# Performance work log

Hardware: AMD Instinct MI355X
Metric: run time of the kernel (lower is better)

## Reference

```python
import jax, jax.numpy as jnp
import numpy as np

E, TOP_K, D, H = 8, 2, 1024, 2048


def setup_inputs() -> dict:
    key = jax.random.key(0)
    ks = jax.random.split(key, 9)
    s = 0.02
    inputs = jax.random.normal(ks[0], (2, 2048, D), dtype=jnp.float32)
    gate_w = jax.random.normal(ks[1], (E, D), dtype=jnp.float32) * s  # Linear(d->E), no bias
    W0 = jax.random.normal(ks[2], (E, D, H), dtype=jnp.float32) * s
    b0 = jnp.zeros((E, H), dtype=jnp.float32)
    W1 = jax.random.normal(ks[3], (E, D, H), dtype=jnp.float32) * s
    b1 = jnp.zeros((E, H), dtype=jnp.float32)
    W2 = jax.random.normal(ks[4], (E, H, D), dtype=jnp.float32) * s
    b2 = jnp.zeros((E, D), dtype=jnp.float32)
    return {"inputs": inputs, "gate_w": gate_w, "W0": W0, "b0": b0,
            "W1": W1, "b1": b1, "W2": W2, "b2": b2}


def reference(inputs, gate_w, W0, b0, W1, b1, W2, b2):
    shp = inputs.shape
    x = inputs.reshape(-1, shp[-1])                      # [T, D]
    T = x.shape[0]
    logits = x @ gate_w.T                                # [T, E]
    w, sel = jax.lax.top_k(logits, TOP_K)                # [T, K]
    w = jax.nn.softmax(w, axis=-1)
    # dense combine weights [T, E]; top-k indices are distinct per row
    combine = jnp.zeros((T, E), dtype=x.dtype).at[
        jnp.arange(T)[:, None], sel].set(w)
    # per-expert SwiGLU FFN, evaluated densely, combined with (mostly zero) weights
    h0 = jnp.einsum('td,edh->eth', x, W0) + b0[:, None, :]
    h1 = jnp.einsum('td,edh->eth', x, W1) + b1[:, None, :]
    y = jnp.einsum('eth,ehd->etd', h0 * jax.nn.silu(h1), W2) + b2[:, None, :]
    out = jnp.einsum('te,etd->td', combine, y)           # [T, D]
    return out.reshape(shp)
```

## Files before the change

### kernel.cpp

```cpp
#include <hip/hip_runtime.h>
#include <hip/hip_bf16.h>
#include <cstdint>


#define E_ 8
#define D_ 1024
#define H_ 2048
#define T_ 4096

typedef __attribute__((ext_vector_type(8))) __bf16 bf16x8;
typedef __attribute__((ext_vector_type(4))) float f32x4;
typedef unsigned short u16;
typedef __attribute__((ext_vector_type(4))) u16 u16x4;

__device__ __forceinline__ u16 f2b(float f) {
    union { float f; unsigned int u; } v; v.f = f;
    unsigned int u = v.u;
    return (u16)((u + 0x7FFFu + ((u >> 16) & 1u)) >> 16);
}

__device__ __forceinline__ float b2f(u16 v) {
    union { unsigned int u; float f; } x; x.u = (unsigned int)v << 16; return x.f;
}

__device__ __forceinline__ void gld16(const void* g, void* l) {
    __builtin_amdgcn_global_load_lds((const __attribute__((address_space(1))) void*)g,
                                     (__attribute__((address_space(3))) void*)l, 16, 0, 0);
}

__global__ void k_gate(const float* __restrict__ x, const float* __restrict__ gw,
                       int* __restrict__ cnt2, int4* __restrict__ tslot,
                       float2* __restrict__ twgt, u16* __restrict__ xb) {
    __shared__ float gws[E_ * D_];
    int tid = threadIdx.x;
#pragma unroll
    for (int p = 0; p < 8; ++p) {
        int i = (p * 256 + tid) * 4;
        *(float4*)&gws[i] = *(const float4*)&gw[i];
    }
    __syncthreads();
    int wid = tid >> 6, lane = tid & 63;
    int t = blockIdx.x * 4 + wid;
    int chunk = blockIdx.x & 63;
    const float* xr = x + (size_t)t * D_;
    float part[E_];
#pragma unroll
    for (int e = 0; e < E_; ++e) part[e] = 0.f;
#pragma unroll
    for (int i = 0; i < 4; ++i) {
        int d = i * 256 + lane * 4;
        float4 xv = *(const float4*)(xr + d);
        u16x4 o;
        o[0] = f2b(xv.x); o[1] = f2b(xv.y); o[2] = f2b(xv.z); o[3] = f2b(xv.w);
        *(u16x4*)(xb + (size_t)t * D_ + d) = o;
#pragma unroll
        for (int e = 0; e < E_; ++e) {
            float4 g = *(const float4*)&gws[e * D_ + d];
            part[e] += xv.x * g.x + xv.y * g.y + xv.z * g.z + xv.w * g.w;
        }
    }
#pragma unroll
    for (int off = 32; off >= 1; off >>= 1) {
#pragma unroll
        for (int e = 0; e < E_; ++e) part[e] += __shfl_xor(part[e], off);
    }
    if (lane == 0) {
        int e0 = 0; float m0 = part[0];
#pragma unroll
        for (int e = 1; e < E_; ++e) if (part[e] > m0) { m0 = part[e]; e0 = e; }
        int e1 = -1; float m1 = -3.4e38f;
#pragma unroll
        for (int e = 0; e < E_; ++e) if (e != e0 && part[e] > m1) { m1 = part[e]; e1 = e; }
        float sx = __expf(m1 - m0);
        float w0 = 1.f / (1.f + sx);
        float w1 = sx / (1.f + sx);
        int lp0 = atomicAdd(&cnt2[chunk * 16 + e0], 1);
        int lp1 = atomicAdd(&cnt2[chunk * 16 + e1], 1);
        tslot[t] = make_int4(e0, lp0, e1, lp1);
        twgt[t] = make_float2(w0, w1);
    }
}

__global__ void k_scan2(const int* __restrict__ cnt2, int* __restrict__ chunk_off,
                        int* __restrict__ cnt, int* __restrict__ offs) {
    __shared__ int totals[E_];
    int e = threadIdx.x >> 6, lane = threadIdx.x & 63;
    int v = cnt2[lane * 16 + e];
    int incl = v;
#pragma unroll
    for (int d = 1; d < 64; d <<= 1) {
        int u = __shfl_up(incl, d);
        if (lane >= d) incl += u;
    }
    int excl = incl - v;
    if (lane == 63) totals[e] = incl;
    __syncthreads();
    chunk_off[lane * 8 + e] = excl;
    if (lane == 0) {
        int off_e = 0;
        for (int q = 0; q < e; ++q) off_e += totals[q];
        offs[e] = off_e; cnt[e] = totals[e];
    }
}

__global__ void k_fixup(const int* __restrict__ chunk_off, int4* __restrict__ tslot,
                        int* __restrict__ tok) {
    int t = blockIdx.x * 256 + threadIdx.x;
    int chunk = (t >> 2) & 63;
    int4 r = tslot[t];
    int s0 = chunk_off[chunk * 8 + r.x] + r.y;
    int s1 = chunk_off[chunk * 8 + r.z] + r.w;
    tok[r.x * T_ + s0] = t;
    tok[r.z * T_ + s1] = t;
    tslot[t] = make_int4(r.x, s0, r.z, s1);
}

__global__ void k_transpose_all(const float* __restrict__ W0, const float* __restrict__ W1,
                                const float* __restrict__ W2, u16* __restrict__ w0t,
                                u16* __restrict__ w1t, u16* __restrict__ w2t) {
    __shared__ float tile[64][67];
    int z = blockIdx.z, which = z >> 3, e = z & 7;
    const float* src; u16* dst; int R, C, c0, r0;
    if (which == 0)      { src = W0 + (size_t)e * D_ * H_; dst = w0t + (size_t)e * D_ * H_;
                           R = D_; C = H_; c0 = blockIdx.x * 64; r0 = blockIdx.y * 64; }
    else if (which == 1) { src = W1 + (size_t)e * D_ * H_; dst = w1t + (size_t)e * D_ * H_;
                           R = D_; C = H_; c0 = blockIdx.x * 64; r0 = blockIdx.y * 64; }
    else                 { src = W2 + (size_t)e * H_ * D_; dst = w2t + (size_t)e * H_ * D_;
                           R = H_; C = D_; c0 = blockIdx.y * 64; r0 = blockIdx.x * 64; }
    int tc4 = (threadIdx.x & 15) * 4, tr = threadIdx.x >> 4;
#pragma unroll
    for (int p = 0; p < 4; ++p) {
        float4 v = *(const float4*)(src + (size_t)(r0 + tr + 16 * p) * C + c0 + tc4);
        tile[tr + 16 * p][tc4 + 0] = v.x;
        tile[tr + 16 * p][tc4 + 1] = v.y;
        tile[tr + 16 * p][tc4 + 2] = v.z;
        tile[tr + 16 * p][tc4 + 3] = v.w;
    }
    __syncthreads();
    int r4 = (threadIdx.x & 15) * 4, tc = threadIdx.x >> 4;
#pragma unroll
    for (int p = 0; p < 4; ++p) {
        int c = tc + 16 * p;
        u16x4 o;
#pragma unroll
        for (int j = 0; j < 4; ++j) o[j] = f2b(tile[r4 + j][c]);
        *(u16x4*)(dst + (size_t)(c0 + c) * R + r0 + r4) = o;
    }
}

__launch_bounds__(256, 2)
__global__ void k_gemm1(const u16* __restrict__ xb, const u16* __restrict__ w0t,
                        const u16* __restrict__ w1t, const float* __restrict__ b0,
                        const float* __restrict__ b1, const int* __restrict__ tok,
                        const int* __restrict__ cnt, const int* __restrict__ offs,
                        u16* __restrict__ gbuf) {
    int e = blockIdx.z, rt = blockIdx.y, ct = blockIdx.x;
    int cN = cnt[e];
    if (rt * 128 >= cN) return;
    __shared__ u16 lds[16384];
    char* ldsB = (char*)lds;
    int tid = threadIdx.x, wid = tid >> 6, lane = tid & 63;
    int wm = wid >> 1, wn = wid & 1;
    const int* tokE = tok + e * T_;
    const u16* w0e = w0t + (size_t)e * H_ * D_;
    const u16* w1e = w1t + (size_t)e * H_ * D_;

    size_t aoff[4]; int adst[4];
#pragma unroll
    for (int p = 0; p < 4; ++p) {
        int cid = p * 256 + tid, r = cid >> 3, c = cid & 7;
        int cc = c ^ (r & 7);
        int tk = tokE[min(rt * 128 + r, cN - 1)];
        aoff[p] = (size_t)tk * D_ + cc * 8;
        adst[p] = (p * 256 + wid * 64) * 16;
    }
    size_t boff[2]; int bdst[2];
#pragma unroll
    for (int p = 0; p < 2; ++p) {
        int cid = p * 256 + tid, n = cid >> 3, c = cid & 7;
        int cc = c ^ (n & 7);
        boff[p] = (size_t)(ct * 64 + n) * D_ + cc * 8;
        bdst[p] = (p * 256 + wid * 64) * 16;
    }

    f32x4 acc0[4][2], acc1[4][2];
#pragma unroll
    for (int m = 0; m < 4; ++m)
#pragma unroll
        for (int n = 0; n < 2; ++n) { acc0[m][n] = (f32x4)0.f; acc1[m][n] = (f32x4)0.f; }

    for (int kt = 0; kt < D_ / 64; ++kt) {
        int k0 = kt * 64;
        __syncthreads();
#pragma unroll
        for (int p = 0; p < 4; ++p) gld16(xb + aoff[p] + k0, ldsB + adst[p]);
#pragma unroll
        for (int p = 0; p < 2; ++p) gld16(w0e + boff[p] + k0, ldsB + 16384 + bdst[p]);
#pragma unroll
        for (int p = 0; p < 2; ++p) gld16(w1e + boff[p] + k0, ldsB + 24576 + bdst[p]);
        __syncthreads();
#pragma unroll
        for (int ks = 0; ks < 2; ++ks) {
            int kc = ks * 4 + (lane >> 4);
            bf16x8 af[4], b0f[2], b1f[2];
#pragma unroll
            for (int m = 0; m < 4; ++m) {
                int row = wm * 64 + m * 16 + (lane & 15);
                af[m] = *(const bf16x8*)(ldsB + row * 128 + ((kc ^ (row & 7)) << 4));
            }
#pragma unroll
            for (int n = 0; n < 2; ++n) {
                int nr = wn * 32 + n * 16 + (lane & 15);
                int so = (kc ^ (nr & 7)) << 4;
                b0f[n] = *(const bf16x8*)(ldsB + 16384 + nr * 128 + so);
                b1f[n] = *(const bf16x8*)(ldsB + 24576 + nr * 128 + so);
            }
#pragma unroll
            for (int m = 0; m < 4; ++m)
#pragma unroll
                for (int n = 0; n < 2; ++n) {
                    acc0[m][n] = __builtin_amdgcn_mfma_f32_16x16x32_bf16(af[m], b0f[n], acc0[m][n], 0, 0, 0);
                    acc1[m][n] = __builtin_amdgcn_mfma_f32_16x16x32_bf16(af[m], b1f[n], acc1[m][n], 0, 0, 0);
                }
        }
    }
    int off_e = offs[e];
    const float* b0e = b0 + e * H_;
    const float* b1e = b1 + e * H_;
#pragma unroll
    for (int n = 0; n < 2; ++n) {
        int hc = ct * 64 + wn * 32 + n * 16 + (lane & 15);
        float bb0 = b0e[hc], bb1 = b1e[hc];
#pragma unroll
        for (int m = 0; m < 4; ++m)
#pragma unroll
            for (int i = 0; i < 4; ++i) {
                int row = wm * 64 + m * 16 + (lane >> 4) * 4 + i;
                int idx = rt * 128 + row;
                if (idx < cN) {
                    float h0 = acc0[m][n][i] + bb0;
                    float h1 = acc1[m][n][i] + bb1;
                    float g = h0 * h1 / (1.f + __expf(-h1));
                    gbuf[(size_t)(off_e + idx) * H_ + hc] = f2b(g);
                }
            }
    }
}

__launch_bounds__(256, 2)
__global__ void k_gemm2(const u16* __restrict__ gbuf, const u16* __restrict__ w2t,
                        const float* __restrict__ b2, const int* __restrict__ cnt,
                        const int* __restrict__ offs, u16* __restrict__ yb) {
    int e = blockIdx.z, rt = blockIdx.y, ct = blockIdx.x;
    int cN = cnt[e];
    if (rt * 128 >= cN) return;
    __shared__ u16 lds[16384];
    char* ldsB = (char*)lds;
    int tid = threadIdx.x, wid = tid >> 6, lane = tid & 63;
    int wm = wid >> 1, wn = wid & 1;
    int off_e = offs[e];
    const u16* Ag = gbuf + (size_t)(off_e + rt * 128) * H_;
    const u16* Bw = w2t + (size_t)e * D_ * H_ + (size_t)(ct * 128) * H_;

    size_t soff[4]; int sdst[4];
#pragma unroll
    for (int p = 0; p < 4; ++p) {
        int cid = p * 256 + tid, r = cid >> 3, c = cid & 7;
        int cc = c ^ (r & 7);
        soff[p] = (size_t)r * H_ + cc * 8;
        sdst[p] = (p * 256 + wid * 64) * 16;
    }
    f32x4 acc[4][4];
#pragma unroll
    for (int m = 0; m < 4; ++m)
#pragma unroll
        for (int n = 0; n < 4; ++n) acc[m][n] = (f32x4)0.f;

    for (int kt = 0; kt < H_ / 64; ++kt) {
        int k0 = kt * 64;
        __syncthreads();
#pragma unroll
        for (int p = 0; p < 4; ++p) gld16(Ag + soff[p] + k0, ldsB + sdst[p]);
#pragma unroll
        for (int p = 0; p < 4; ++p) gld16(Bw + soff[p] + k0, ldsB + 16384 + sdst[p]);
        __syncthreads();
#pragma unroll
        for (int ks = 0; ks < 2; ++ks) {
            int kc = ks * 4 + (lane >> 4);
            bf16x8 af[4], bfr[4];
#pragma unroll
            for (int m = 0; m < 4; ++m) {
                int row = wm * 64 + m * 16 + (lane & 15);
                af[m] = *(const bf16x8*)(ldsB + row * 128 + ((kc ^ (row & 7)) << 4));
            }
#pragma unroll
            for (int n = 0; n < 4; ++n) {
                int nr = wn * 64 + n * 16 + (lane & 15);
                bfr[n] = *(const bf16x8*)(ldsB + 16384 + nr * 128 + ((kc ^ (nr & 7)) << 4));
            }
#pragma unroll
            for (int m = 0; m < 4; ++m)
#pragma unroll
                for (int n = 0; n < 4; ++n)
                    acc[m][n] = __builtin_amdgcn_mfma_f32_16x16x32_bf16(af[m], bfr[n], acc[m][n], 0, 0, 0);
        }
    }
    const float* b2e = b2 + e * D_;
#pragma unroll
    for (int m = 0; m < 4; ++m)
#pragma unroll
        for (int i = 0; i < 4; ++i) {
            int row = wm * 64 + m * 16 + (lane >> 4) * 4 + i;
            int idx = rt * 128 + row;
            if (idx < cN) {
#pragma unroll
                for (int n = 0; n < 4; ++n) {
                    int dc = ct * 128 + wn * 64 + n * 16 + (lane & 15);
                    yb[(size_t)(off_e + idx) * D_ + dc] = f2b(acc[m][n][i] + b2e[dc]);
                }
            }
        }
}

__global__ void k_combine(const u16* __restrict__ yb, const int4* __restrict__ tslot,
                          const float2* __restrict__ twgt, const int* __restrict__ offs,
                          float* __restrict__ out) {
    int t = blockIdx.x, d4 = threadIdx.x * 4;
    int4 s = tslot[t];
    float2 w = twgt[t];
    const u16* y0 = yb + (size_t)(offs[s.x] + s.y) * D_ + d4;
    const u16* y1 = yb + (size_t)(offs[s.z] + s.w) * D_ + d4;
    u16x4 a = *(const u16x4*)y0;
    u16x4 b = *(const u16x4*)y1;
    float4 o;
    o.x = w.x * b2f(a[0]) + w.y * b2f(b[0]);
    o.y = w.x * b2f(a[1]) + w.y * b2f(b[1]);
    o.z = w.x * b2f(a[2]) + w.y * b2f(b[2]);
    o.w = w.x * b2f(a[3]) + w.y * b2f(b[3]);
    *(float4*)(out + (size_t)t * D_ + d4) = o;
}

extern "C" void kernel_launch(void* const* d_in, const int* in_sizes, int n_in,
                              void* d_out, int out_size, void* d_ws, size_t ws_size,
                              hipStream_t stream) {
    const float* x  = (const float*)d_in[0];
    const float* gw = (const float*)d_in[1];
    const float* W0 = (const float*)d_in[2];
    const float* b0 = (const float*)d_in[3];
    const float* W1 = (const float*)d_in[4];
    const float* b1 = (const float*)d_in[5];
    const float* W2 = (const float*)d_in[6];
    const float* b2 = (const float*)d_in[7];
    float* out = (float*)d_out;

    char* ws = (char*)d_ws;
    size_t off = 0;
    u16* xb   = (u16*)(ws + off); off += (size_t)T_ * D_ * 2;
    u16* w0t  = (u16*)(ws + off); off += (size_t)E_ * H_ * D_ * 2;
    u16* w1t  = (u16*)(ws + off); off += (size_t)E_ * H_ * D_ * 2;
    u16* w2t  = (u16*)(ws + off); off += (size_t)E_ * D_ * H_ * 2;
    u16* gbuf = (u16*)(ws + off); off += (size_t)(T_ * 2 + 256) * H_ * 2;
    int*   tok   = (int*)(ws + off);    off += (size_t)E_ * T_ * 4;
    int4*  tslot = (int4*)(ws + off);   off += (size_t)T_ * 16;
    float2* twgt = (float2*)(ws + off); off += (size_t)T_ * 8;
    int*   cnt2  = (int*)(ws + off);    off += 64 * 16 * 4;
    int*   choff = (int*)(ws + off);    off += 64 * 8 * 4;
    int*   cnt   = (int*)(ws + off);    off += 64;
    int*   offs  = (int*)(ws + off);    off += 64;
    u16* yb = w0t;

    if (ws_size < off) return;
    hipMemsetAsync(cnt2, 0, 64 * 16 * 4, stream);

    k_gate<<<T_ / 4, 256, 0, stream>>>(x, gw, cnt2, tslot, twgt, xb);
    k_scan2<<<1, 512, 0, stream>>>(cnt2, choff, cnt, offs);
    k_fixup<<<T_ / 256, 256, 0, stream>>>(choff, tslot, tok);
    k_transpose_all<<<dim3(32, 16, 24), 256, 0, stream>>>(W0, W1, W2, w0t, w1t, w2t);
    k_gemm1<<<dim3(H_ / 64, T_ / 128, E_), 256, 0, stream>>>(xb, w0t, w1t, b0, b1, tok, cnt, offs, gbuf);
    k_gemm2<<<dim3(D_ / 128, T_ / 128, E_), 256, 0, stream>>>(gbuf, w2t, b2, cnt, offs, yb);
    k_combine<<<T_, 256, 0, stream>>>(yb, tslot, twgt, offs, out);
}
```

Measured before the change: 239.5 us.

## Double-buffer LDS K-tiles in both expert GEMMs with async global loads

Both grouped GEMM kernels switch from a single 64-wide K tile loaded and consumed between two __syncthreads to a two-stage ring of 32-wide K tiles. The next tile's global-to-LDS loads are issued before the current tile is computed, and explicit vmcnt waits plus raw s_barrier replace the full syncs. The aim is to hide global load latency behind MFMA work. In exchange there are twice as many barriers per K, a new XOR swizzle for 64-byte rows, and reliance on hand-counted vmcnt values being correct.

Result: slower. 263.8 us (+10.2%).

```diff
diff --git a/kernel.cpp b/kernel.cpp
--- a/kernel.cpp
+++ b/kernel.cpp
@@ -157,31 +157,33 @@
     int e = blockIdx.z, rt = blockIdx.y, ct = blockIdx.x;
     int cN = cnt[e];
     if (rt * 128 >= cN) return;
-    __shared__ u16 lds[16384];
-    char* ldsB = (char*)lds;
+    __shared__ char ldsB[32768];
     int tid = threadIdx.x, wid = tid >> 6, lane = tid & 63;
     int wm = wid >> 1, wn = wid & 1;
     const int* tokE = tok + e * T_;
     const u16* w0e = w0t + (size_t)e * H_ * D_;
     const u16* w1e = w1t + (size_t)e * H_ * D_;
 
-    size_t aoff[4]; int adst[4];
-#pragma unroll
-    for (int p = 0; p < 4; ++p) {
-        int cid = p * 256 + tid, r = cid >> 3, c = cid & 7;
-        int cc = c ^ (r & 7);
+    size_t aoff[2]; int adst[2];
+#pragma unroll
+    for (int p = 0; p < 2; ++p) {
+        int cid = p * 256 + tid, r = cid >> 2, c = cid & 3;
+        int cc = c ^ ((r >> 1) & 3);
         int tk = tokE[min(rt * 128 + r, cN - 1)];
         aoff[p] = (size_t)tk * D_ + cc * 8;
         adst[p] = (p * 256 + wid * 64) * 16;
     }
-    size_t boff[2]; int bdst[2];
-#pragma unroll
-    for (int p = 0; p < 2; ++p) {
-        int cid = p * 256 + tid, n = cid >> 3, c = cid & 7;
-        int cc = c ^ (n & 7);
-        boff[p] = (size_t)(ct * 64 + n) * D_ + cc * 8;
-        bdst[p] = (p * 256 + wid * 64) * 16;
-    }
+    int nB = tid >> 2, cB = tid & 3, ccB = cB ^ ((nB >> 1) & 3);
+    size_t b0off = (size_t)(ct * 64 + nB) * D_ + ccB * 8;
+    int bdst = (wid * 64) * 16;
+
+    auto stage = [&](int buf, int k0) {
+        char* S = ldsB + buf * 16384;
+        gld16(xb + aoff[0] + k0, S + adst[0]);
+        gld16(xb + aoff[1] + k0, S + adst[1]);
+        gld16(w0e + b0off + k0, S + 8192 + bdst);
+        gld16(w1e + b0off + k0, S + 12288 + bdst);
+    };
 
     f32x4 acc0[4][2], acc1[4][2];
 #pragma unroll
@@ -189,41 +191,39 @@
 #pragma unroll
         for (int n = 0; n < 2; ++n) { acc0[m][n] = (f32x4)0.f; acc1[m][n] = (f32x4)0.f; }
 
-    for (int kt = 0; kt < D_ / 64; ++kt) {
-        int k0 = kt * 64;
-        __syncthreads();
-#pragma unroll
-        for (int p = 0; p < 4; ++p) gld16(xb + aoff[p] + k0, ldsB + adst[p]);
-#pragma unroll
-        for (int p = 0; p < 2; ++p) gld16(w0e + boff[p] + k0, ldsB + 16384 + bdst[p]);
-#pragma unroll
-        for (int p = 0; p < 2; ++p) gld16(w1e + boff[p] + k0, ldsB + 24576 + bdst[p]);
-        __syncthreads();
-#pragma unroll
-        for (int ks = 0; ks < 2; ++ks) {
-            int kc = ks * 4 + (lane >> 4);
-            bf16x8 af[4], b0f[2], b1f[2];
-#pragma unroll
-            for (int m = 0; m < 4; ++m) {
-                int row = wm * 64 + m * 16 + (lane & 15);
-                af[m] = *(const bf16x8*)(ldsB + row * 128 + ((kc ^ (row & 7)) << 4));
+    const int NT = D_ / 32;
+    stage(0, 0);
+    stage(1, 32);
+    for (int t = 0; t < NT; ++t) {
+        if (t + 1 < NT) asm volatile("s_waitcnt vmcnt(4)" ::: "memory");
+        else            asm volatile("s_waitcnt vmcnt(0)" ::: "memory");
+        __builtin_amdgcn_s_barrier();
+        const char* S = ldsB + (t & 1) * 16384;
+        int kc = lane >> 4;
+        bf16x8 af[4], b0f[2], b1f[2];
+#pragma unroll
+        for (int m = 0; m < 4; ++m) {
+            int row = wm * 64 + m * 16 + (lane & 15);
+            af[m] = *(const bf16x8*)(S + row * 64 + ((kc ^ ((row >> 1) & 3)) << 4));
+        }
+#pragma unroll
+        for (int n = 0; n < 2; ++n) {
+            int nr = wn * 32 + n * 16 + (lane & 15);
+            int so = (kc ^ ((nr >> 1) & 3)) << 4;
+            b0f[n] = *(const bf16x8*)(S + 8192 + nr * 64 + so);
+            b1f[n] = *(const bf16x8*)(S + 12288 + nr * 64 + so);
+        }
+#pragma unroll
+        for (int m = 0; m < 4; ++m)
+#pragma unroll
+            for (int n = 0; n < 2; ++n) {
+                acc0[m][n] = __builtin_amdgcn_mfma_f32_16x16x32_bf16(af[m], b0f[n], acc0[m][n], 0, 0, 0);
+                acc1[m][n] = __builtin_amdgcn_mfma_f32_16x16x32_bf16(af[m], b1f[n], acc1[m][n], 0, 0, 0);
             }
-#pragma unroll
-            for (int n = 0; n < 2; ++n) {
-                int nr = wn * 32 + n * 16 + (lane & 15);
-                int so = (kc ^ (nr & 7)) << 4;
-                b0f[n] = *(const bf16x8*)(ldsB + 16384 + nr * 128 + so);
-                b1f[n] = *(const bf16x8*)(ldsB + 24576 + nr * 128 + so);
-            }
-#pragma unroll
-            for (int m = 0; m < 4; ++m)
-#pragma unroll
-                for (int n = 0; n < 2; ++n) {
-                    acc0[m][n] = __builtin_amdgcn_mfma_f32_16x16x32_bf16(af[m], b0f[n], acc0[m][n], 0, 0, 0);
-                    acc1[m][n] = __builtin_amdgcn_mfma_f32_16x16x32_bf16(af[m], b1f[n], acc1[m][n], 0, 0, 0);
-                }
-        }
-    }
+        __builtin_amdgcn_s_barrier();
+        if (t + 2 < NT) stage(t & 1, (t + 2) * 32);
+    }
+
     int off_e = offs[e];
     const float* b0e = b0 + e * H_;
     const float* b1e = b1 + e * H_;
@@ -254,57 +254,65 @@
     int e = blockIdx.z, rt = blockIdx.y, ct = blockIdx.x;
     int cN = cnt[e];
     if (rt * 128 >= cN) return;
-    __shared__ u16 lds[16384];
-    char* ldsB = (char*)lds;
+    __shared__ char ldsB[32768];
     int tid = threadIdx.x, wid = tid >> 6, lane = tid & 63;
     int wm = wid >> 1, wn = wid & 1;
     int off_e = offs[e];
     const u16* Ag = gbuf + (size_t)(off_e + rt * 128) * H_;
     const u16* Bw = w2t + (size_t)e * D_ * H_ + (size_t)(ct * 128) * H_;
 
-    size_t soff[4]; int sdst[4];
-#pragma unroll
-    for (int p = 0; p < 4; ++p) {
-        int cid = p * 256 + tid, r = cid >> 3, c = cid & 7;
-        int cc = c ^ (r & 7);
+    size_t soff[2]; int sdst[2];
+#pragma unroll
+    for (int p = 0; p < 2; ++p) {
+        int cid = p * 256 + tid, r = cid >> 2, c = cid & 3;
+        int cc = c ^ ((r >> 1) & 3);
         soff[p] = (size_t)r * H_ + cc * 8;
         sdst[p] = (p * 256 + wid * 64) * 16;
     }
+
+    auto stage = [&](int buf, int k0) {
+        char* S = ldsB + buf * 16384;
+        gld16(Ag + soff[0] + k0, S + sdst[0]);
+        gld16(Ag + soff[1] + k0, S + sdst[1]);
+        gld16(Bw + soff[0] + k0, S + 8192 + sdst[0]);
+        gld16(Bw + soff[1] + k0, S + 8192 + sdst[1]);
+    };
+
     f32x4 acc[4][4];
 #pragma unroll
     for (int m = 0; m < 4; ++m)
 #pragma unroll
         for (int n = 0; n < 4; ++n) acc[m][n] = (f32x4)0.f;
 
-    for (int kt = 0; kt < H_ / 64; ++kt) {
-        int k0 = kt * 64;
-        __syncthreads();
-#pragma unroll
-        for (int p = 0; p < 4; ++p) gld16(Ag + soff[p] + k0, ldsB + sdst[p]);
-#pragma unroll
-        for (int p = 0; p < 4; ++p) gld16(Bw + soff[p] + k0, ldsB + 16384 + sdst[p]);
-        __syncthreads();
-#pragma unroll
-        for (int ks = 0; ks < 2; ++ks) {
-            int kc = ks * 4 + (lane >> 4);
-            bf16x8 af[4], bfr[4];
-#pragma unroll
-            for (int m = 0; m < 4; ++m) {
-                int row = wm * 64 + m * 16 + (lane & 15);
-                af[m] = *(const bf16x8*)(ldsB + row * 128 + ((kc ^ (row & 7)) << 4));
-            }
-#pragma unroll
-            for (int n = 0; n < 4; ++n) {
-                int nr = wn * 64 + n * 16 + (lane & 15);
-                bfr[n] = *(const bf16x8*)(ldsB + 16384 + nr * 128 + ((kc ^ (nr & 7)) << 4));
-            }
-#pragma unroll
-            for (int m = 0; m < 4; ++m)
-#pragma unroll
-                for (int n = 0; n < 4; ++n)
-                    acc[m][n] = __builtin_amdgcn_mfma_f32_16x16x32_bf16(af[m], bfr[n], acc[m][n], 0, 0, 0);
-        }
-    }
+    const int NT = H_ / 32;
+    stage(0, 0);
+    stage(1, 32);
+    for (int t = 0; t < NT; ++t) {
+        if (t + 1 < NT) asm volatile("s_waitcnt vmcnt(4)" ::: "memory");
+        else            asm volatile("s_waitcnt vmcnt(0)" ::: "memory");
+        __builtin_amdgcn_s_barrier();
+        const char* S = ldsB + (t & 1) * 16384;
+        int kc = lane >> 4;
+        bf16x8 af[4], bfr[4];
+#pragma unroll
+        for (int m = 0; m < 4; ++m) {
+            int row = wm * 64 + m * 16 + (lane & 15);
+            af[m] = *(const bf16x8*)(S + row * 64 + ((kc ^ ((row >> 1) & 3)) << 4));
+        }
+#pragma unroll
+        for (int n = 0; n < 4; ++n) {
+            int nr = wn * 64 + n * 16 + (lane & 15);
+            bfr[n] = *(const bf16x8*)(S + 8192 + nr * 64 + ((kc ^ ((nr >> 1) & 3)) << 4));
+        }
+#pragma unroll
+        for (int m = 0; m < 4; ++m)
+#pragma unroll
+            for (int n = 0; n < 4; ++n)
+                acc[m][n] = __builtin_amdgcn_mfma_f32_16x16x32_bf16(af[m], bfr[n], acc[m][n], 0, 0, 0);
+        __builtin_amdgcn_s_barrier();
+        if (t + 2 < NT) stage(t & 1, (t + 2) * 32);
+    }
+
     const float* b2e = b2 + e * D_;
 #pragma unroll
     for (int m = 0; m < 4; ++m)
```

## Rewrite gate/up GEMM as 256x128 tile, 8-wave, double-buffered pipelined kernel

Applied to the files above, without the earlier changes.

The first expert GEMM now uses 512-thread blocks, each computing a 256-row by 128-column tile (64 gate plus 64 up columns interleaved in one B tile). The kernel double-buffers LDS at 128 KB and splits each k-step into four quadrant phases. Each phase issues the next stage's global-to-LDS loads, waits on vmcnt, and hits a barrier, while s_setprio raises priority around the MFMA bursts. The aim is to overlap memory loads with matrix math and get more reuse per load. In exchange it uses a large LDS footprint and more accumulator registers, which limits occupancy, and it relies on fragile hand-counted waitcnts. Row tiles are also coarser, which wastes more work on the padded tail of each expert.

After: 251.1 us. +4.8%, slower.

```diff
diff --git a/kernel.cpp b/kernel.cpp
--- a/kernel.cpp
+++ b/kernel.cpp
@@ -148,7 +148,7 @@
     }
 }
 
-__launch_bounds__(256, 2)
+__launch_bounds__(512, 2)
 __global__ void k_gemm1(const u16* __restrict__ xb, const u16* __restrict__ w0t,
                         const u16* __restrict__ w1t, const float* __restrict__ b0,
                         const float* __restrict__ b1, const int* __restrict__ tok,
@@ -156,90 +156,135 @@
                         u16* __restrict__ gbuf) {
     int e = blockIdx.z, rt = blockIdx.y, ct = blockIdx.x;
     int cN = cnt[e];
-    if (rt * 128 >= cN) return;
-    __shared__ u16 lds[16384];
-    char* ldsB = (char*)lds;
+    if (rt * 256 >= cN) return;
+    __shared__ char lds[131072];
     int tid = threadIdx.x, wid = tid >> 6, lane = tid & 63;
-    int wm = wid >> 1, wn = wid & 1;
+    int wm = wid >> 2, wn = wid & 3;
     const int* tokE = tok + e * T_;
     const u16* w0e = w0t + (size_t)e * H_ * D_;
-    const u16* w1e = w1t + (size_t)e * H_ * D_;
-
-    size_t aoff[4]; int adst[4];
-#pragma unroll
-    for (int p = 0; p < 4; ++p) {
-        int cid = p * 256 + tid, r = cid >> 3, c = cid & 7;
-        int cc = c ^ (r & 7);
-        int tk = tokE[min(rt * 128 + r, cN - 1)];
-        aoff[p] = (size_t)tk * D_ + cc * 8;
-        adst[p] = (p * 256 + wid * 64) * 16;
-    }
-    size_t boff[2]; int bdst[2];
-#pragma unroll
-    for (int p = 0; p < 2; ++p) {
-        int cid = p * 256 + tid, n = cid >> 3, c = cid & 7;
-        int cc = c ^ (n & 7);
-        boff[p] = (size_t)(ct * 64 + n) * D_ + cc * 8;
-        bdst[p] = (p * 256 + wid * 64) * 16;
-    }
-
-    f32x4 acc0[4][2], acc1[4][2];
-#pragma unroll
-    for (int m = 0; m < 4; ++m)
-#pragma unroll
-        for (int n = 0; n < 2; ++n) { acc0[m][n] = (f32x4)0.f; acc1[m][n] = (f32x4)0.f; }
-
-    for (int kt = 0; kt < D_ / 64; ++kt) {
-        int k0 = kt * 64;
-        __syncthreads();
-#pragma unroll
-        for (int p = 0; p < 4; ++p) gld16(xb + aoff[p] + k0, ldsB + adst[p]);
-#pragma unroll
-        for (int p = 0; p < 2; ++p) gld16(w0e + boff[p] + k0, ldsB + 16384 + bdst[p]);
-#pragma unroll
-        for (int p = 0; p < 2; ++p) gld16(w1e + boff[p] + k0, ldsB + 24576 + bdst[p]);
-        __syncthreads();
+    size_t wdelta = (size_t)(w1t - w0t);
+
+    unsigned aoff[4]; int adst[4];
+#pragma unroll
+    for (int i = 0; i < 4; ++i) {
+        int cid = i * 512 + tid;
+        int r = cid >> 3, c = cid & 7, cc = c ^ (r & 7);
+        int tk = tokE[min(rt * 256 + r, cN - 1)];
+        aoff[i] = (unsigned)(tk * D_ + cc * 8);
+        adst[i] = (i * 512 + wid * 64) * 16;
+    }
+    size_t boff[2][2]; int bdst[2][2];
+#pragma unroll
+    for (int NH = 0; NH < 2; ++NH)
+#pragma unroll
+        for (int l = 0; l < 2; ++l) {
+            int c = l * 512 + tid;
+            int rw = c >> 3;
+            int q = rw >> 5;
+            int rr = (q * 2 + NH) * 32 + (rw & 31);
+            int cc = (c & 7) ^ (rr & 7);
+            int g = rr >> 5, which = g & 1;
+            int hcol = ct * 128 + (g >> 1) * 32 + (rr & 31);
+            boff[NH][l] = (size_t)which * wdelta + (size_t)hcol * D_ + cc * 8;
+            int rw0 = l * 64 + wid * 8;
+            int rr0 = ((rw0 >> 5) * 2 + NH) * 32 + (rw0 & 31);
+            bdst[NH][l] = 32768 + rr0 * 128;
+        }
+
+    auto stA = [&](int MH, char* slot, int k0) {
+        gld16(xb + aoff[MH] + k0, slot + adst[MH]);
+        gld16(xb + aoff[MH + 2] + k0, slot + adst[MH + 2]);
+    };
+    auto stB = [&](int NH, char* slot, int k0) {
+        gld16(w0e + boff[NH][0] + k0, slot + bdst[NH][0]);
+        gld16(w0e + boff[NH][1] + k0, slot + bdst[NH][1]);
+    };
+
+    f32x4 acc[8][4];
+#pragma unroll
+    for (int m = 0; m < 8; ++m)
+#pragma unroll
+        for (int n = 0; n < 4; ++n) acc[m][n] = (f32x4)0.f;
+
+    auto rdA = [&](const char* As, int MH, bf16x8 (&af)[2][4]) {
 #pragma unroll
         for (int ks = 0; ks < 2; ++ks) {
             int kc = ks * 4 + (lane >> 4);
-            bf16x8 af[4], b0f[2], b1f[2];
 #pragma unroll
             for (int m = 0; m < 4; ++m) {
-                int row = wm * 64 + m * 16 + (lane & 15);
-                af[m] = *(const bf16x8*)(ldsB + row * 128 + ((kc ^ (row & 7)) << 4));
-            }
+                int row = wm * 128 + MH * 64 + m * 16 + (lane & 15);
+                af[ks][m] = *(const bf16x8*)(As + row * 128 + ((kc ^ (row & 7)) << 4));
+            }
+        }
+    };
+    auto rdB = [&](const char* Bs, int NH, bf16x8 (&bf)[2][2]) {
+#pragma unroll
+        for (int ks = 0; ks < 2; ++ks) {
+            int kc = ks * 4 + (lane >> 4);
 #pragma unroll
             for (int n = 0; n < 2; ++n) {
-                int nr = wn * 32 + n * 16 + (lane & 15);
-                int so = (kc ^ (nr & 7)) << 4;
-                b0f[n] = *(const bf16x8*)(ldsB + 16384 + nr * 128 + so);
-                b1f[n] = *(const bf16x8*)(ldsB + 24576 + nr * 128 + so);
-            }
+                int rb = wn * 64 + (NH * 2 + n) * 16 + (lane & 15);
+                bf[ks][n] = *(const bf16x8*)(Bs + rb * 128 + ((kc ^ (rb & 7)) << 4));
+            }
+        }
+    };
+    auto mfma = [&](int MH, int NH, bf16x8 (&af)[2][4], bf16x8 (&bf)[2][2]) {
+        __builtin_amdgcn_s_setprio(1);
+#pragma unroll
+        for (int ks = 0; ks < 2; ++ks)
 #pragma unroll
             for (int m = 0; m < 4; ++m)
 #pragma unroll
-                for (int n = 0; n < 2; ++n) {
-                    acc0[m][n] = __builtin_amdgcn_mfma_f32_16x16x32_bf16(af[m], b0f[n], acc0[m][n], 0, 0, 0);
-                    acc1[m][n] = __builtin_amdgcn_mfma_f32_16x16x32_bf16(af[m], b1f[n], acc1[m][n], 0, 0, 0);
-                }
-        }
-    }
+                for (int n = 0; n < 2; ++n)
+                    acc[MH * 4 + m][NH * 2 + n] = __builtin_amdgcn_mfma_f32_16x16x32_bf16(
+                        af[ks][m], bf[ks][n], acc[MH * 4 + m][NH * 2 + n], 0, 0, 0);
+        __builtin_amdgcn_s_setprio(0);
+    };
+
+    const int NT = D_ / 64;
+    stA(0, lds, 0); stB(0, lds, 0); stA(1, lds, 0); stB(1, lds, 0);
+    for (int t = 0; t < NT; ++t) {
+        char* As = lds + (t & 1) * 65536;
+        char* Bs = As + 32768;
+        char* Ns = lds + ((t + 1) & 1) * 65536;
+        int k1 = (t + 1) * 64;
+        bool pf = (t + 1 < NT);
+        bf16x8 a0[2][4], a1[2][4], bq0[2][2], bq1[2][2];
+        asm volatile("s_waitcnt vmcnt(4)" ::: "memory");
+        __builtin_amdgcn_s_barrier();
+        rdA(As, 0, a0); rdB(Bs, 0, bq0);
+        if (pf) stA(0, Ns, k1);
+        mfma(0, 0, a0, bq0);
+        if (pf) asm volatile("s_waitcnt vmcnt(4)" ::: "memory");
+        else    asm volatile("s_waitcnt vmcnt(2)" ::: "memory");
+        __builtin_amdgcn_s_barrier();
+        rdA(As, 1, a1);
+        if (pf) stB(0, Ns, k1);
+        mfma(1, 0, a1, bq0);
+        if (pf) asm volatile("s_waitcnt vmcnt(4)" ::: "memory");
+        else    asm volatile("s_waitcnt vmcnt(0)" ::: "memory");
+        __builtin_amdgcn_s_barrier();
+        rdB(Bs, 1, bq1);
+        if (pf) stA(1, Ns, k1);
+        mfma(0, 1, a0, bq1);
+        __builtin_amdgcn_s_barrier();
+        if (pf) stB(1, Ns, k1);
+        mfma(1, 1, a1, bq1);
+    }
+
     int off_e = offs[e];
-    const float* b0e = b0 + e * H_;
-    const float* b1e = b1 + e * H_;
 #pragma unroll
     for (int n = 0; n < 2; ++n) {
-        int hc = ct * 64 + wn * 32 + n * 16 + (lane & 15);
-        float bb0 = b0e[hc], bb1 = b1e[hc];
-#pragma unroll
-        for (int m = 0; m < 4; ++m)
+        int hc = ct * 128 + wn * 32 + n * 16 + (lane & 15);
+        float bb0 = b0[e * H_ + hc], bb1 = b1[e * H_ + hc];
+#pragma unroll
+        for (int mi = 0; mi < 8; ++mi)
 #pragma unroll
             for (int i = 0; i < 4; ++i) {
-                int row = wm * 64 + m * 16 + (lane >> 4) * 4 + i;
-                int idx = rt * 128 + row;
+                int idx = rt * 256 + wm * 128 + mi * 16 + (lane >> 4) * 4 + i;
                 if (idx < cN) {
-                    float h0 = acc0[m][n][i] + bb0;
-                    float h1 = acc1[m][n][i] + bb1;
+                    float h0 = acc[mi][n][i] + bb0;
+                    float h1 = acc[mi][n + 2][i] + bb1;
                     float g = h0 * h1 / (1.f + __expf(-h1));
                     gbuf[(size_t)(off_e + idx) * H_ + hc] = f2b(g);
                 }
@@ -376,7 +421,7 @@
     k_scan2<<<1, 512, 0, stream>>>(cnt2, choff, cnt, offs);
     k_fixup<<<T_ / 256, 256, 0, stream>>>(choff, tslot, tok);
     k_transpose_all<<<dim3(32, 16, 24), 256, 0, stream>>>(W0, W1, W2, w0t, w1t, w2t);
-    k_gemm1<<<dim3(H_ / 64, T_ / 128, E_), 256, 0, stream>>>(xb, w0t, w1t, b0, b1, tok, cnt, offs, gbuf);
+    k_gemm1<<<dim3(H_ / 128, T_ / 256, E_), 512, 0, stream>>>(xb, w0t, w1t, b0, b1, tok, cnt, offs, gbuf);
     k_gemm2<<<dim3(D_ / 128, T_ / 128, E_), 256, 0, stream>>>(gbuf, w2t, b2, cnt, offs, yb);
     k_combine<<<T_, 256, 0, stream>>>(yb, tslot, twgt, offs, out);
 }
```
